# Kernel tuning notes

Hardware: AMD Instinct MI355X
Metric: run time of the kernel (lower is better)

The kernel has to match this reference:

```python
import jax, jax.numpy as jnp
import numpy as np

N, F_IN, C0, C1, H, E, G = 50000, 128, 64, 64, 4, 800000, 256
NEG_SLOPE = 0.2
BN_EPS = 1e-5


def setup_inputs() -> dict:
    key = jax.random.key(0)
    ks = jax.random.split(key, 16)
    d = {
        'x': jax.random.normal(ks[0], (N, F_IN), dtype=jnp.float32),
        'edge_index': jax.random.randint(ks[1], (2, E), 0, N, dtype=jnp.int64),
        'batch': jnp.sort(jax.random.randint(ks[2], (N,), 0, G, dtype=jnp.int64)),
        # conv1 params
        'W1': jax.random.normal(ks[3], (F_IN, H * C0), dtype=jnp.float32) * (1.0 / np.sqrt(F_IN)),
        'att_src1': jax.random.normal(ks[4], (H, C0), dtype=jnp.float32) * 0.1,
        'att_dst1': jax.random.normal(ks[5], (H, C0), dtype=jnp.float32) * 0.1,
        'b1': jnp.zeros((H * C0,), dtype=jnp.float32),
        # batchnorm params
        'gamma': jnp.ones((H * C0,), dtype=jnp.float32),
        'beta': jnp.zeros((H * C0,), dtype=jnp.float32),
        # conv2 params
        'W2': jax.random.normal(ks[6], (H * C0, H * C1), dtype=jnp.float32) * (1.0 / np.sqrt(H * C0)),
        'att_src2': jax.random.normal(ks[7], (H, C1), dtype=jnp.float32) * 0.1,
        'att_dst2': jax.random.normal(ks[8], (H, C1), dtype=jnp.float32) * 0.1,
        'b2': jnp.zeros((H * C1,), dtype=jnp.float32),
    }
    return d


def _gat_layer(x, W, a_src, a_dst, b, src, dst, heads, ch):
    # x: [N, Fin] -> h: [N, H, C]
    h = (x @ W).reshape(N, heads, ch)
    al_src = jnp.sum(h * a_src, axis=-1)  # [N, H]
    al_dst = jnp.sum(h * a_dst, axis=-1)  # [N, H]
    e = jax.nn.leaky_relu(al_src[src] + al_dst[dst], NEG_SLOPE)  # [E', H]
    m = jax.ops.segment_max(e, dst, num_segments=N)
    m = jnp.where(jnp.isfinite(m), m, 0.0)
    ex = jnp.exp(e - m[dst])
    denom = jax.ops.segment_sum(ex, dst, num_segments=N)
    alpha = ex / (denom[dst] + 1e-16)  # softmax over in-neighborhood of dst
    out = jax.ops.segment_sum(alpha[:, :, None] * h[src], dst, num_segments=N)  # [N, H, C]
    return out.reshape(N, heads * ch) + b


def _batchnorm(x, gamma, beta):
    mu = jnp.mean(x, axis=0)
    var = jnp.var(x, axis=0)
    return gamma * (x - mu) / jnp.sqrt(var + BN_EPS) + beta


def reference(x, edge_index, batch, W1, att_src1, att_dst1, b1, gamma, beta,
              W2, att_src2, att_dst2, b2):
    # add self loops (PyG GATConv default)
    loops = jnp.arange(N, dtype=edge_index.dtype)
    src = jnp.concatenate([edge_index[0], loops])
    dst = jnp.concatenate([edge_index[1], loops])

    x1 = _gat_layer(x, W1, att_src1, att_dst1, b1, src, dst, H, C0)
    x1 = jax.nn.relu(_batchnorm(x1, gamma, beta))
    x2 = jax.nn.relu(_gat_layer(x1, W2, att_src2, att_dst2, b2, src, dst, H, C1))

    xc = jnp.concatenate([x1, x2], axis=1)  # [N, H*C0 + H*C1]
    counts = jax.ops.segment_sum(jnp.ones((N,), xc.dtype), batch, num_segments=G)
    x_mean = jax.ops.segment_sum(xc, batch, num_segments=G) / jnp.maximum(counts, 1.0)[:, None]
    x_max = jax.ops.segment_max(xc, batch, num_segments=G)
    x_max = jnp.where(jnp.isfinite(x_max), x_max, 0.0)
    return jnp.concatenate([x_mean, x_max], axis=1)  # [G, 2*(H*C0+H*C1)]
```

## Files before the change

kernel.cpp:

```cpp
#include <hip/hip_runtime.h>
#include <hip/hip_bf16.h>
#include <math.h>

#define NN 50000
#define FIN 128
#define FH 256
#define NE 800000
#define NG 256
#define ELLS 64
#define NEG_SLOPE 0.2f
#define BN_EPS 1e-5f

typedef short bf16x8 __attribute__((ext_vector_type(8)));
typedef unsigned short u16x8 __attribute__((ext_vector_type(8)));
typedef unsigned long long u64x2 __attribute__((ext_vector_type(2)));
typedef float f32x4 __attribute__((ext_vector_type(4)));

__device__ __forceinline__ float lrelu(float x) { return x > 0.f ? x : NEG_SLOPE * x; }
__device__ __forceinline__ float bf2f(unsigned short u) { return __uint_as_float(((unsigned int)u) << 16); }
__device__ __forceinline__ unsigned short f2bf(float f) {
    __hip_bfloat16 b = __float2bfloat16(f);
    return *reinterpret_cast<unsigned short*>(&b);
}

__global__ __launch_bounds__(256) void k_prep(const float* __restrict__ W1, unsigned short* __restrict__ W1t,
                                              const float* __restrict__ W2, unsigned short* __restrict__ W2t,
                                              int* __restrict__ cnt, int* __restrict__ colIdx) {
    int bid = blockIdx.x;
    if (bid < 384) {
        int o = bid * 256 + threadIdx.x;
        if (o < 256 * 128) {
            int c = o >> 7, k = o & 127;
            W1t[o] = f2bf(W1[(size_t)k * 256 + c]);
        } else {
            o -= 256 * 128;
            if (o < 256 * 256) {
                int c = o >> 8, k = o & 255;
                W2t[o] = f2bf(W2[(size_t)k * 256 + c]);
            }
        }
    } else {
        int i = (bid - 384) * 256 + threadIdx.x;
        if (i < NN) {
            cnt[i] = 1;
            colIdx[(size_t)i * ELLS] = i;
        }
    }
}

template<int MODE>
__global__ __launch_bounds__(256) void k_gemm(const float* __restrict__ Af, const unsigned short* __restrict__ Ab,
                                              const unsigned short* __restrict__ Bt,
                                              unsigned short* __restrict__ C,
                                              const float* __restrict__ attS, const float* __restrict__ attD,
                                              float* __restrict__ alsrc, float* __restrict__ aldst,
                                              const float* __restrict__ bnsum, const float* __restrict__ bnsq,
                                              const float* __restrict__ gamma, const float* __restrict__ beta,
                                              const int* __restrict__ eiFill, int* __restrict__ cntFill,
                                              int* __restrict__ colIdxFill, int nGemm,
                                              int M, int K) {
    __shared__ short lds[10240];
    __shared__ float sAs_[128], sAd_[128];
    __shared__ float s_scale[MODE == 1 ? 256 : 1];
    __shared__ float s_shift[MODE == 1 ? 256 : 1];
    short* As = lds;
    short* Bs = lds + 5120;

    int bid = blockIdx.x;
    if (MODE == 0 && bid >= nGemm) {
        int i = (bid - nGemm) * 256 + threadIdx.x;
        if (i < NE) {
            int s = eiFill[i], d = eiFill[NE + i];
            int pos = atomicAdd(&cntFill[d], 1);
            if (pos < ELLS) colIdxFill[(size_t)d * ELLS + pos] = s;
        }
        return;
    }
    int tid = threadIdx.x;
    int lane = tid & 63, wid = tid >> 6;
    int wr = wid >> 1, wc = wid & 1;
    int row0 = (bid >> 1) * 128, col0 = (bid & 1) * 128;

    if (tid < 128) {
        sAs_[tid] = attS[col0 + tid];
        sAd_[tid] = attD[col0 + tid];
    }
    if (MODE == 1) {
        const float invN = 1.f / (float)NN;
        float mean = bnsum[tid] * invN;
        float var  = bnsq[tid] * invN - mean * mean;
        float istd = rsqrtf(var + BN_EPS);
        float sc = gamma[tid] * istd;
        s_scale[tid] = sc;
        s_shift[tid] = beta[tid] - mean * sc;
        __syncthreads();
    }
    f32x4 acc[4][4];
#pragma unroll
    for (int m = 0; m < 4; ++m)
#pragma unroll
        for (int n = 0; n < 4; ++n) acc[m][n] = (f32x4){0.f, 0.f, 0.f, 0.f};

    int r = tid >> 2, seg = tid & 3;
    int koff = (lane >> 4) * 8;

    float4 qa0[2], qa1[2];
    bf16x8 qab[2];
    bf16x8 qb[2];
    const float4 zf4 = make_float4(0.f, 0.f, 0.f, 0.f);
    const bf16x8 zb8 = {0, 0, 0, 0, 0, 0, 0, 0};

#pragma unroll
    for (int j = 0; j < 2; ++j) {
        int grow = row0 + r + j * 64;
        if (MODE == 0) {
            if (grow < M) {
                const float* ap = Af + (size_t)grow * K + seg * 8;
                qa0[j] = *(const float4*)ap;
                qa1[j] = *((const float4*)ap + 1);
            } else { qa0[j] = zf4; qa1[j] = zf4; }
        } else {
            qab[j] = (grow < M) ? *(const bf16x8*)(Ab + (size_t)grow * K + seg * 8) : zb8;
        }
        qb[j] = *(const bf16x8*)(Bt + (size_t)(col0 + r + j * 64) * K + seg * 8);
    }

    for (int k0 = 0; k0 < K; k0 += 32) {
#pragma unroll
        for (int j = 0; j < 2; ++j) {
            int row = r + j * 64;
            bf16x8 va;
            if (MODE == 0) {
                va[0] = (short)f2bf(qa0[j].x); va[1] = (short)f2bf(qa0[j].y);
                va[2] = (short)f2bf(qa0[j].z); va[3] = (short)f2bf(qa0[j].w);
                va[4] = (short)f2bf(qa1[j].x); va[5] = (short)f2bf(qa1[j].y);
                va[6] = (short)f2bf(qa1[j].z); va[7] = (short)f2bf(qa1[j].w);
            } else {
                int cb = k0 + seg * 8;
#pragma unroll
                for (int k = 0; k < 8; ++k) {
                    float f = bf2f((unsigned short)qab[j][k]) * s_scale[cb + k] + s_shift[cb + k];
                    va[k] = (short)f2bf(fmaxf(f, 0.f));
                }
            }
            *(bf16x8*)&As[row * 40 + seg * 8] = va;
            *(bf16x8*)&Bs[row * 40 + seg * 8] = qb[j];
        }
        __syncthreads();
        int kn = k0 + 32;
        if (kn < K) {
#pragma unroll
            for (int j = 0; j < 2; ++j) {
                int grow = row0 + r + j * 64;
                if (MODE == 0) {
                    if (grow < M) {
                        const float* ap = Af + (size_t)grow * K + kn + seg * 8;
                        qa0[j] = *(const float4*)ap;
                        qa1[j] = *((const float4*)ap + 1);
                    } else { qa0[j] = zf4; qa1[j] = zf4; }
                } else {
                    qab[j] = (grow < M) ? *(const bf16x8*)(Ab + (size_t)grow * K + kn + seg * 8) : zb8;
                }
                qb[j] = *(const bf16x8*)(Bt + (size_t)(col0 + r + j * 64) * K + kn + seg * 8);
            }
        }
        bf16x8 af[4], bfr[4];
#pragma unroll
        for (int m = 0; m < 4; ++m)
            af[m] = *(const bf16x8*)&As[(wr * 64 + m * 16 + (lane & 15)) * 40 + koff];
#pragma unroll
        for (int n = 0; n < 4; ++n)
            bfr[n] = *(const bf16x8*)&Bs[(wc * 64 + n * 16 + (lane & 15)) * 40 + koff];
#pragma unroll
        for (int m = 0; m < 4; ++m)
#pragma unroll
            for (int n = 0; n < 4; ++n)
                acc[m][n] = __builtin_amdgcn_mfma_f32_16x16x32_bf16(af[m], bfr[n], acc[m][n], 0, 0, 0);
        __syncthreads();
    }

    const int CST = 138;
#pragma unroll 1
    for (int hh = 0; hh < 2; ++hh) {
        if (wr == hh) {
#pragma unroll
            for (int m = 0; m < 4; ++m) {
                int rl = m * 16 + (lane >> 4) * 4;
#pragma unroll
                for (int n = 0; n < 4; ++n) {
                    int cl = wc * 64 + n * 16 + (lane & 15);
#pragma unroll
                    for (int j = 0; j < 4; ++j)
                        lds[(rl + j) * CST + cl] = (short)f2bf(acc[m][n][j]);
                }
            }
        }
        __syncthreads();
        int rl = tid >> 2, q = tid & 3;
        int grow = row0 + hh * 64 + rl;
        if (grow < M) {
            const short* cp = &lds[rl * CST + q * 32];
            bf16x8 v0 = *(const bf16x8*)(cp + 0);
            bf16x8 v1 = *(const bf16x8*)(cp + 8);
            bf16x8 v2 = *(const bf16x8*)(cp + 16);
            bf16x8 v3 = *(const bf16x8*)(cp + 24);
            unsigned short* op = C + (size_t)grow * 256 + col0 + q * 32;
            *(bf16x8*)(op + 0)  = v0;
            *(bf16x8*)(op + 8)  = v1;
            *(bf16x8*)(op + 16) = v2;
            *(bf16x8*)(op + 24) = v3;
            float ps = 0.f, pd = 0.f;
            const float* aS = &sAs_[q * 32];
            const float* aD = &sAd_[q * 32];
#pragma unroll
            for (int k = 0; k < 8; ++k) {
                float f0 = bf2f((unsigned short)v0[k]);
                float f1 = bf2f((unsigned short)v1[k]);
                float f2 = bf2f((unsigned short)v2[k]);
                float f3 = bf2f((unsigned short)v3[k]);
                ps += f0 * aS[k] + f1 * aS[k + 8] + f2 * aS[k + 16] + f3 * aS[k + 24];
                pd += f0 * aD[k] + f1 * aD[k + 8] + f2 * aD[k + 16] + f3 * aD[k + 24];
            }
            ps += __shfl_xor(ps, 1);
            pd += __shfl_xor(pd, 1);
            if ((q & 1) == 0) {
                int head = (col0 >> 6) + (q >> 1);
                alsrc[grow * 4 + head] = ps;
                aldst[grow * 4 + head] = pd;
            }
        }
        __syncthreads();
    }
}

__global__ __launch_bounds__(256) void k_gat_agg(const int* __restrict__ cnt, const int* __restrict__ colIdx,
    const float* __restrict__ alsrc, const float* __restrict__ aldst, const unsigned short* __restrict__ h,
    const float* __restrict__ bias, unsigned short* __restrict__ outb, int relu_nt, int n) {
    __shared__ float ex_s[4][2][32][4];
    __shared__ int   src_s[4][2][32];
    int wave = threadIdx.x >> 6, lane = threadIdx.x & 63;
    int half = lane >> 5, hlane = lane & 31;
    int node = blockIdx.x * 8 + wave * 2 + half;
    int deg = min(cnt[node], ELLS);
    const int* crow = colIdx + (size_t)node * ELLS;
    int hf = hlane >> 3;
    float4 ad = *(const float4*)(aldst + (size_t)node * 4);
    float m0 = -1e30f, m1 = -1e30f, m2 = -1e30f, m3 = -1e30f;
    float d0 = 0.f, d1 = 0.f, d2 = 0.f, d3 = 0.f;
    float acc[8];
#pragma unroll
    for (int k = 0; k < 8; ++k) acc[k] = 0.f;

    for (int base = 0; base < deg; base += 32) {
        int cnt32 = min(32, deg - base);
        int src = node;
        float e0 = -1e30f, e1 = -1e30f, e2 = -1e30f, e3 = -1e30f;
        if (hlane < cnt32) {
            src = crow[base + hlane];
            float4 as = *(const float4*)(alsrc + (size_t)src * 4);
            e0 = lrelu(as.x + ad.x);
            e1 = lrelu(as.y + ad.y);
            e2 = lrelu(as.z + ad.z);
            e3 = lrelu(as.w + ad.w);
        }
        float c0 = e0, c1 = e1, c2 = e2, c3 = e3;
#pragma unroll
        for (int off = 16; off > 0; off >>= 1) {
            c0 = fmaxf(c0, __shfl_xor(c0, off));
            c1 = fmaxf(c1, __shfl_xor(c1, off));
            c2 = fmaxf(c2, __shfl_xor(c2, off));
            c3 = fmaxf(c3, __shfl_xor(c3, off));
        }
        float nm0 = fmaxf(m0, c0), nm1 = fmaxf(m1, c1), nm2 = fmaxf(m2, c2), nm3 = fmaxf(m3, c3);
        float sc0 = __expf(m0 - nm0), sc1 = __expf(m1 - nm1), sc2 = __expf(m2 - nm2), sc3 = __expf(m3 - nm3);
        float x0 = __expf(e0 - nm0), x1 = __expf(e1 - nm1), x2 = __expf(e2 - nm2), x3 = __expf(e3 - nm3);
        float s0 = x0, s1 = x1, s2 = x2, s3 = x3;
#pragma unroll
        for (int off = 16; off > 0; off >>= 1) {
            s0 += __shfl_xor(s0, off);
            s1 += __shfl_xor(s1, off);
            s2 += __shfl_xor(s2, off);
            s3 += __shfl_xor(s3, off);
        }
        d0 = d0 * sc0 + s0; d1 = d1 * sc1 + s1; d2 = d2 * sc2 + s2; d3 = d3 * sc3 + s3;
        m0 = nm0; m1 = nm1; m2 = nm2; m3 = nm3;
        float scl = (hf == 0) ? sc0 : (hf == 1) ? sc1 : (hf == 2) ? sc2 : sc3;
#pragma unroll
        for (int k = 0; k < 8; ++k) acc[k] *= scl;
        ex_s[wave][half][hlane][0] = x0; ex_s[wave][half][hlane][1] = x1;
        ex_s[wave][half][hlane][2] = x2; ex_s[wave][half][hlane][3] = x3;
        src_s[wave][half][hlane] = src;
        for (int j = 0; j < cnt32; j += 2) {
            float w0 = ex_s[wave][half][j][hf];
            bf16x8 h0 = *(const bf16x8*)(h + (size_t)src_s[wave][half][j] * 256 + hlane * 8);
            float w1 = 0.f;
            bf16x8 h1 = {0, 0, 0, 0, 0, 0, 0, 0};
            if (j + 1 < cnt32) {
                w1 = ex_s[wave][half][j + 1][hf];
                h1 = *(const bf16x8*)(h + (size_t)src_s[wave][half][j + 1] * 256 + hlane * 8);
            }
#pragma unroll
            for (int k = 0; k < 8; ++k)
                acc[k] = fmaf(w0, bf2f((unsigned short)h0[k]), acc[k]);
#pragma unroll
            for (int k = 0; k < 8; ++k)
                acc[k] = fmaf(w1, bf2f((unsigned short)h1[k]), acc[k]);
        }
    }

    float dd = (hf == 0) ? d0 : (hf == 1) ? d1 : (hf == 2) ? d2 : d3;
    float inv = 1.f / (dd + 1e-16f);
    float4 b0 = *(const float4*)(bias + hlane * 8);
    float4 b1 = *(const float4*)(bias + hlane * 8 + 4);
    float o[8];
    o[0] = acc[0] * inv + b0.x; o[1] = acc[1] * inv + b0.y;
    o[2] = acc[2] * inv + b0.z; o[3] = acc[3] * inv + b0.w;
    o[4] = acc[4] * inv + b1.x; o[5] = acc[5] * inv + b1.y;
    o[6] = acc[6] * inv + b1.z; o[7] = acc[7] * inv + b1.w;
    u16x8 ob;
    if (relu_nt) {
#pragma unroll
        for (int k = 0; k < 8; ++k) ob[k] = f2bf(fmaxf(o[k], 0.f));
        u64x2 w = *(u64x2*)&ob;
        __builtin_nontemporal_store(w, (u64x2*)(outb + (size_t)node * 256 + hlane * 8));
    } else {
#pragma unroll
        for (int k = 0; k < 8; ++k) ob[k] = f2bf(o[k]);
        *(u64x2*)(outb + (size_t)node * 256 + hlane * 8) = *(u64x2*)&ob;
    }
}

__global__ __launch_bounds__(256) void k_bn_stats(const unsigned short* __restrict__ xin, float* bnsum, float* bnsq) {
    int t = threadIdx.x;
    int r0 = blockIdx.x * 250;
    float s = 0.f, q = 0.f;
    for (int r = r0; r < r0 + 250; ++r) {
        float v = bf2f(xin[(size_t)r * 256 + t]);
        s += v; q += v * v;
    }
    atomicAdd(&bnsum[t], s);
    atomicAdd(&bnsq[t], q);
}

__global__ __launch_bounds__(512) void k_pool(const unsigned short* __restrict__ x1pre,
    const unsigned short* __restrict__ x2b, const int* __restrict__ batch,
    const float* __restrict__ bnsum, const float* __restrict__ bnsq,
    const float* __restrict__ gamma, const float* __restrict__ beta,
    float* __restrict__ out) {
    int g = blockIdx.x;
    __shared__ int sLo, sHi;
    if (threadIdx.x == 0) {
        int lo = 0, hi = NN;
        while (lo < hi) { int m = (lo + hi) >> 1; if (batch[m] < g) lo = m + 1; else hi = m; }
        sLo = lo;
    }
    if (threadIdx.x == 1) {
        int lo = 0, hi = NN;
        while (lo < hi) { int m = (lo + hi) >> 1; if (batch[m] < g + 1) lo = m + 1; else hi = m; }
        sHi = lo;
    }
    __syncthreads();
    int lo = sLo, hi = sHi, cnt = hi - lo;
    int t = threadIdx.x;
    bool first = t < 256;
    int f = first ? t : t - 256;
    const unsigned short* src = first ? x1pre : x2b;
    float sc = 1.f, sh = 0.f;
    if (first) {
        const float invN = 1.f / (float)NN;
        float mean = bnsum[f] * invN;
        float var  = bnsq[f] * invN - mean * mean;
        float istd = rsqrtf(var + BN_EPS);
        sc = gamma[f] * istd;
        sh = beta[f] - mean * sc;
    }
    float s = 0.f, mx = 0.f;
    int r = lo;
    for (; r + 1 < hi; r += 2) {
        float va = bf2f(src[(size_t)r * 256 + f]);
        float vb = bf2f(src[(size_t)(r + 1) * 256 + f]);
        if (first) {
            va = fmaxf(va * sc + sh, 0.f);
            vb = fmaxf(vb * sc + sh, 0.f);
        }
        s += va + vb;
        mx = fmaxf(mx, fmaxf(va, vb));
    }
    if (r < hi) {
        float va = bf2f(src[(size_t)r * 256 + f]);
        if (first) va = fmaxf(va * sc + sh, 0.f);
        s += va; mx = fmaxf(mx, va);
    }
    float mean = (cnt > 0) ? s / (float)cnt : 0.f;
    int off = first ? 0 : 256;
    out[g * 1024 + off + f] = mean;
    out[g * 1024 + 512 + off + f] = mx;
}

extern "C" void kernel_launch(void* const* d_in, const int* in_sizes, int n_in,
                              void* d_out, int out_size, void* d_ws, size_t ws_size,
                              hipStream_t stream) {
    const float* x     = (const float*)d_in[0];
    const int*   ei    = (const int*)d_in[1];
    const int*   batch = (const int*)d_in[2];
    const float* W1    = (const float*)d_in[3];
    const float* asrc1 = (const float*)d_in[4];
    const float* adst1 = (const float*)d_in[5];
    const float* b1    = (const float*)d_in[6];
    const float* gamma = (const float*)d_in[7];
    const float* beta  = (const float*)d_in[8];
    const float* W2    = (const float*)d_in[9];
    const float* asrc2 = (const float*)d_in[10];
    const float* adst2 = (const float*)d_in[11];
    const float* b2    = (const float*)d_in[12];
    float* out = (float*)d_out;

    char* p = (char*)d_ws;
    auto alloc = [&](size_t bytes) -> void* {
        void* r = (void*)p;
        p += (bytes + 255) & ~(size_t)255;
        return r;
    };
    unsigned short* hb    = (unsigned short*)alloc((size_t)NN * 256 * 2);
    unsigned short* x1pre = (unsigned short*)alloc((size_t)NN * 256 * 2);
    unsigned short* x2b   = (unsigned short*)alloc((size_t)NN * 256 * 2);
    unsigned short* W1t   = (unsigned short*)alloc((size_t)256 * 128 * 2);
    unsigned short* W2t   = (unsigned short*)alloc((size_t)256 * 256 * 2);
    float* alsrc = (float*)alloc((size_t)NN * 4 * 4);
    float* aldst = (float*)alloc((size_t)NN * 4 * 4);
    float* bnsum = (float*)alloc(256 * 4);
    float* bnsq  = (float*)alloc(256 * 4);
    int*   cnt   = (int*)alloc((size_t)NN * 4);
    int*   colIdx = (int*)alloc((size_t)NN * ELLS * 4);

    (void)hipMemsetAsync(bnsum, 0, 2 * 1024, stream);

    const int nbE = (NE + 255) / 256;
    const int nGemm = 2 * ((NN + 127) / 128);

    k_prep<<<384 + 196, 256, 0, stream>>>(W1, W1t, W2, W2t, cnt, colIdx);

    k_gemm<0><<<nGemm + nbE, 256, 0, stream>>>(x, nullptr, W1t, hb, asrc1, adst1, alsrc, aldst,
                                               nullptr, nullptr, nullptr, nullptr,
                                               ei, cnt, colIdx, nGemm, NN, 128);
    k_gat_agg<<<NN / 8, 256, 0, stream>>>(cnt, colIdx, alsrc, aldst, hb, b1, x1pre, 0, NN);
    k_bn_stats<<<200, 256, 0, stream>>>(x1pre, bnsum, bnsq);

    k_gemm<1><<<nGemm, 256, 0, stream>>>(nullptr, x1pre, W2t, hb, asrc2, adst2, alsrc, aldst,
                                         bnsum, bnsq, gamma, beta,
                                         nullptr, nullptr, nullptr, nGemm, NN, 256);
    k_gat_agg<<<NN / 8, 256, 0, stream>>>(cnt, colIdx, alsrc, aldst, hb, b2, x2b, 1, NN);

    k_pool<<<NG, 512, 0, stream>>>(x1pre, x2b, batch, bnsum, bnsq, gamma, beta, out);
}
```

Baseline: 293.3 us.

## Use fp16 features and packed fp16 accumulation, batch edge fill, vectorize BN stats

The GEMM epilogue now stores features as fp16 instead of bf16, and the aggregation kernel accumulates in packed fp16 vectors (f16x8 multiply-add) rather than converting each element to fp32 for FMA. The point is to cut ALU work in the gather-heavy aggregation loop. Separately, the edge-fill blocks each handle four edges per thread so their loads and atomics overlap, and the BN stats kernel switches to 16-byte vector loads with an LDS reduction. The cost is precision: accumulating in fp16 and scaling weights to fp16 can lose accuracy or overflow on large sums.

```diff
diff --git a/kernel.cpp b/kernel.cpp
--- a/kernel.cpp
+++ b/kernel.cpp
@@ -1,5 +1,6 @@
 #include <hip/hip_runtime.h>
 #include <hip/hip_bf16.h>
+#include <hip/hip_fp16.h>
 #include <math.h>
 
 #define NN 50000
@@ -15,12 +16,21 @@
 typedef unsigned short u16x8 __attribute__((ext_vector_type(8)));
 typedef unsigned long long u64x2 __attribute__((ext_vector_type(2)));
 typedef float f32x4 __attribute__((ext_vector_type(4)));
+typedef _Float16 f16x8 __attribute__((ext_vector_type(8)));
 
 __device__ __forceinline__ float lrelu(float x) { return x > 0.f ? x : NEG_SLOPE * x; }
 __device__ __forceinline__ float bf2f(unsigned short u) { return __uint_as_float(((unsigned int)u) << 16); }
 __device__ __forceinline__ unsigned short f2bf(float f) {
     __hip_bfloat16 b = __float2bfloat16(f);
     return *reinterpret_cast<unsigned short*>(&b);
+}
+__device__ __forceinline__ unsigned short f2h(float f) {
+    __half h = __float2half(f);
+    return *reinterpret_cast<unsigned short*>(&h);
+}
+__device__ __forceinline__ float h2f(unsigned short u) {
+    __half_raw r; r.x = u;
+    return __half2float(__half(r));
 }
 
 __global__ __launch_bounds__(256) void k_prep(const float* __restrict__ W1, unsigned short* __restrict__ W1t,
@@ -57,7 +67,7 @@
                                               const float* __restrict__ bnsum, const float* __restrict__ bnsq,
                                               const float* __restrict__ gamma, const float* __restrict__ beta,
                                               const int* __restrict__ eiFill, int* __restrict__ cntFill,
-                                              int* __restrict__ colIdxFill, int nGemm,
+                                              int* __restrict__ colIdxFill, int nGemm, int nFill,
                                               int M, int K) {
     __shared__ short lds[10240];
     __shared__ float sAs_[128], sAd_[128];
@@ -68,12 +78,23 @@
 
     int bid = blockIdx.x;
     if (MODE == 0 && bid >= nGemm) {
-        int i = (bid - nGemm) * 256 + threadIdx.x;
-        if (i < NE) {
-            int s = eiFill[i], d = eiFill[NE + i];
-            int pos = atomicAdd(&cntFill[d], 1);
-            if (pos < ELLS) colIdxFill[(size_t)d * ELLS + pos] = s;
-        }
+        int T = nFill * 256;
+        int t = (bid - nGemm) * 256 + threadIdx.x;
+        int e0 = t, e1 = t + T, e2 = t + 2 * T, e3 = t + 3 * T;
+        int s0 = 0, s1 = 0, s2 = 0, s3 = 0, d0 = -1, d1 = -1, d2 = -1, d3 = -1;
+        if (e0 < NE) { s0 = eiFill[e0]; d0 = eiFill[NE + e0]; }
+        if (e1 < NE) { s1 = eiFill[e1]; d1 = eiFill[NE + e1]; }
+        if (e2 < NE) { s2 = eiFill[e2]; d2 = eiFill[NE + e2]; }
+        if (e3 < NE) { s3 = eiFill[e3]; d3 = eiFill[NE + e3]; }
+        int p0 = 0, p1 = 0, p2 = 0, p3 = 0;
+        if (d0 >= 0) p0 = atomicAdd(&cntFill[d0], 1);
+        if (d1 >= 0) p1 = atomicAdd(&cntFill[d1], 1);
+        if (d2 >= 0) p2 = atomicAdd(&cntFill[d2], 1);
+        if (d3 >= 0) p3 = atomicAdd(&cntFill[d3], 1);
+        if (d0 >= 0 && p0 < ELLS) colIdxFill[(size_t)d0 * ELLS + p0] = s0;
+        if (d1 >= 0 && p1 < ELLS) colIdxFill[(size_t)d1 * ELLS + p1] = s1;
+        if (d2 >= 0 && p2 < ELLS) colIdxFill[(size_t)d2 * ELLS + p2] = s2;
+        if (d3 >= 0 && p3 < ELLS) colIdxFill[(size_t)d3 * ELLS + p3] = s3;
         return;
     }
     int tid = threadIdx.x;
@@ -191,7 +212,7 @@
                     int cl = wc * 64 + n * 16 + (lane & 15);
 #pragma unroll
                     for (int j = 0; j < 4; ++j)
-                        lds[(rl + j) * CST + cl] = (short)f2bf(acc[m][n][j]);
+                        lds[(rl + j) * CST + cl] = (short)f2h(acc[m][n][j]);
                 }
             }
         }
@@ -214,10 +235,10 @@
             const float* aD = &sAd_[q * 32];
 #pragma unroll
             for (int k = 0; k < 8; ++k) {
-                float f0 = bf2f((unsigned short)v0[k]);
-                float f1 = bf2f((unsigned short)v1[k]);
-                float f2 = bf2f((unsigned short)v2[k]);
-                float f3 = bf2f((unsigned short)v3[k]);
+                float f0 = h2f((unsigned short)v0[k]);
+                float f1 = h2f((unsigned short)v1[k]);
+                float f2 = h2f((unsigned short)v2[k]);
+                float f3 = h2f((unsigned short)v3[k]);
                 ps += f0 * aS[k] + f1 * aS[k + 8] + f2 * aS[k + 16] + f3 * aS[k + 24];
                 pd += f0 * aD[k] + f1 * aD[k + 8] + f2 * aD[k + 16] + f3 * aD[k + 24];
             }
@@ -247,9 +268,7 @@
     float4 ad = *(const float4*)(aldst + (size_t)node * 4);
     float m0 = -1e30f, m1 = -1e30f, m2 = -1e30f, m3 = -1e30f;
     float d0 = 0.f, d1 = 0.f, d2 = 0.f, d3 = 0.f;
-    float acc[8];
-#pragma unroll
-    for (int k = 0; k < 8; ++k) acc[k] = 0.f;
+    f16x8 accv = {0, 0, 0, 0, 0, 0, 0, 0};
 
     for (int base = 0; base < deg; base += 32) {
         int cnt32 = min(32, deg - base);
@@ -285,26 +304,28 @@
         d0 = d0 * sc0 + s0; d1 = d1 * sc1 + s1; d2 = d2 * sc2 + s2; d3 = d3 * sc3 + s3;
         m0 = nm0; m1 = nm1; m2 = nm2; m3 = nm3;
         float scl = (hf == 0) ? sc0 : (hf == 1) ? sc1 : (hf == 2) ? sc2 : sc3;
-#pragma unroll
-        for (int k = 0; k < 8; ++k) acc[k] *= scl;
+        {
+            _Float16 sh = (_Float16)scl;
+            f16x8 sv = {sh, sh, sh, sh, sh, sh, sh, sh};
+            accv *= sv;
+        }
         ex_s[wave][half][hlane][0] = x0; ex_s[wave][half][hlane][1] = x1;
         ex_s[wave][half][hlane][2] = x2; ex_s[wave][half][hlane][3] = x3;
         src_s[wave][half][hlane] = src;
         for (int j = 0; j < cnt32; j += 2) {
             float w0 = ex_s[wave][half][j][hf];
-            bf16x8 h0 = *(const bf16x8*)(h + (size_t)src_s[wave][half][j] * 256 + hlane * 8);
+            f16x8 h0 = *(const f16x8*)(h + (size_t)src_s[wave][half][j] * 256 + hlane * 8);
             float w1 = 0.f;
-            bf16x8 h1 = {0, 0, 0, 0, 0, 0, 0, 0};
+            f16x8 h1 = {0, 0, 0, 0, 0, 0, 0, 0};
             if (j + 1 < cnt32) {
                 w1 = ex_s[wave][half][j + 1][hf];
-                h1 = *(const bf16x8*)(h + (size_t)src_s[wave][half][j + 1] * 256 + hlane * 8);
-            }
-#pragma unroll
-            for (int k = 0; k < 8; ++k)
-                acc[k] = fmaf(w0, bf2f((unsigned short)h0[k]), acc[k]);
-#pragma unroll
-            for (int k = 0; k < 8; ++k)
-                acc[k] = fmaf(w1, bf2f((unsigned short)h1[k]), acc[k]);
+                h1 = *(const f16x8*)(h + (size_t)src_s[wave][half][j + 1] * 256 + hlane * 8);
+            }
+            _Float16 w0h = (_Float16)w0, w1h = (_Float16)w1;
+            f16x8 w0v = {w0h, w0h, w0h, w0h, w0h, w0h, w0h, w0h};
+            f16x8 w1v = {w1h, w1h, w1h, w1h, w1h, w1h, w1h, w1h};
+            accv += h0 * w0v;
+            accv += h1 * w1v;
         }
     }
 
@@ -313,10 +334,10 @@
     float4 b0 = *(const float4*)(bias + hlane * 8);
     float4 b1 = *(const float4*)(bias + hlane * 8 + 4);
     float o[8];
-    o[0] = acc[0] * inv + b0.x; o[1] = acc[1] * inv + b0.y;
-    o[2] = acc[2] * inv + b0.z; o[3] = acc[3] * inv + b0.w;
-    o[4] = acc[4] * inv + b1.x; o[5] = acc[5] * inv + b1.y;
-    o[6] = acc[6] * inv + b1.z; o[7] = acc[7] * inv + b1.w;
+    o[0] = (float)accv[0] * inv + b0.x; o[1] = (float)accv[1] * inv + b0.y;
+    o[2] = (float)accv[2] * inv + b0.z; o[3] = (float)accv[3] * inv + b0.w;
+    o[4] = (float)accv[4] * inv + b1.x; o[5] = (float)accv[5] * inv + b1.y;
+    o[6] = (float)accv[6] * inv + b1.z; o[7] = (float)accv[7] * inv + b1.w;
     u16x8 ob;
     if (relu_nt) {
 #pragma unroll
@@ -331,15 +352,28 @@
 }
 
 __global__ __launch_bounds__(256) void k_bn_stats(const unsigned short* __restrict__ xin, float* bnsum, float* bnsq) {
-    int t = threadIdx.x;
-    int r0 = blockIdx.x * 250;
-    float s = 0.f, q = 0.f;
-    for (int r = r0; r < r0 + 250; ++r) {
-        float v = bf2f(xin[(size_t)r * 256 + t]);
-        s += v; q += v * v;
-    }
-    atomicAdd(&bnsum[t], s);
-    atomicAdd(&bnsq[t], q);
+    __shared__ float ls[8][256], lq[8][256];
+    int t = threadIdx.x, cg = t & 31, rg = t >> 5;
+    int r0 = blockIdx.x * 200;
+    float s[8], q[8];
+#pragma unroll
+    for (int k = 0; k < 8; ++k) { s[k] = 0.f; q[k] = 0.f; }
+    for (int r = r0 + rg; r < r0 + 200; r += 8) {
+        u16x8 v = *(const u16x8*)(xin + (size_t)r * 256 + cg * 8);
+#pragma unroll
+        for (int k = 0; k < 8; ++k) {
+            float f = bf2f(v[k]);
+            s[k] += f; q[k] += f * f;
+        }
+    }
+#pragma unroll
+    for (int k = 0; k < 8; ++k) { ls[rg][cg * 8 + k] = s[k]; lq[rg][cg * 8 + k] = q[k]; }
+    __syncthreads();
+    float S = 0.f, Q = 0.f;
+#pragma unroll
+    for (int j = 0; j < 8; ++j) { S += ls[j][t]; Q += lq[j][t]; }
+    atomicAdd(&bnsum[t], S);
+    atomicAdd(&bnsq[t], Q);
 }
 
 __global__ __launch_bounds__(512) void k_pool(const unsigned short* __restrict__ x1pre,
@@ -435,20 +469,20 @@
 
     (void)hipMemsetAsync(bnsum, 0, 2 * 1024, stream);
 
-    const int nbE = (NE + 255) / 256;
     const int nGemm = 2 * ((NN + 127) / 128);
+    const int nFill = (NE / 4 + 255) / 256;
 
     k_prep<<<384 + 196, 256, 0, stream>>>(W1, W1t, W2, W2t, cnt, colIdx);
 
-    k_gemm<0><<<nGemm + nbE, 256, 0, stream>>>(x, nullptr, W1t, hb, asrc1, adst1, alsrc, aldst,
-                                               nullptr, nullptr, nullptr, nullptr,
-                                               ei, cnt, colIdx, nGemm, NN, 128);
+    k_gemm<0><<<nGemm + nFill, 256, 0, stream>>>(x, nullptr, W1t, hb, asrc1, adst1, alsrc, aldst,
+                                                 nullptr, nullptr, nullptr, nullptr,
+                                                 ei, cnt, colIdx, nGemm, nFill, NN, 128);
     k_gat_agg<<<NN / 8, 256, 0, stream>>>(cnt, colIdx, alsrc, aldst, hb, b1, x1pre, 0, NN);
-    k_bn_stats<<<200, 256, 0, stream>>>(x1pre, bnsum, bnsq);
+    k_bn_stats<<<250, 256, 0, stream>>>(x1pre, bnsum, bnsq);
 
     k_gemm<1><<<nGemm, 256, 0, stream>>>(nullptr, x1pre, W2t, hb, asrc2, adst2, alsrc, aldst,
                                          bnsum, bnsq, gamma, beta,
-                                         nullptr, nullptr, nullptr, nGemm, NN, 256);
+                                         nullptr, nullptr, nullptr, nGemm, 0, NN, 256);
     k_gat_agg<<<NN / 8, 256, 0, stream>>>(cnt, colIdx, alsrc, aldst, hb, b2, x2b, 1, NN);
 
     k_pool<<<NG, 512, 0, stream>>>(x1pre, x2b, batch, bnsum, bnsq, gamma, beta, out);
```

After: 284.9 us, median of 2. 1.03x faster.
